# Kernel optimization log

Hardware: AMD Instinct MI355X
Metric: run time of the kernel (lower is better)

The kernel has to match this reference:

```python
import jax, jax.numpy as jnp
import numpy as np

NUM_HEADS = 32
HEAD_DIM = 128
ROPE_DIM = 64
HIDDEN = 4096
C_KV = 512
C_Q = 1536
CACHE_LEN = 4096
BATCH = 4


def _apply_rope(x, positions):
    # x: [B, S, H, R]; interleaved rotate-half RoPE at given absolute positions
    R = x.shape[-1]
    inv_freq = 1.0 / (10000.0 ** (jnp.arange(0, R, 2, dtype=jnp.float32) / R))
    ang = positions[:, None].astype(jnp.float32) * inv_freq[None, :]  # [S, R/2]
    cos = jnp.cos(ang)[None, :, None, :]
    sin = jnp.sin(ang)[None, :, None, :]
    x1, x2 = x[..., 0::2], x[..., 1::2]
    out = jnp.stack([x1 * cos - x2 * sin, x1 * sin + x2 * cos], axis=-1)
    return out.reshape(x.shape).astype(x.dtype)


def setup_inputs() -> dict:
    key = jax.random.key(0)
    ks = jax.random.split(key, 12)
    s = lambda fan: 1.0 / np.sqrt(fan)
    return {
        "hidden_states": jax.random.normal(ks[0], (BATCH, 1, HIDDEN), jnp.float32),
        "mask": jnp.zeros((BATCH, 1, 1, CACHE_LEN + 1), jnp.float32),
        "cached_c_KV": jax.random.normal(ks[1], (BATCH, CACHE_LEN, C_KV), jnp.float32),
        "cached_k_R": jax.random.normal(ks[2], (BATCH, CACHE_LEN, ROPE_DIM), jnp.float32),
        "W_DKV": jax.random.normal(ks[3], (HIDDEN, C_KV), jnp.float32) * s(HIDDEN),
        "W_UK": jax.random.normal(ks[4], (C_KV, NUM_HEADS * HEAD_DIM), jnp.float32) * s(C_KV),
        "W_UV": jax.random.normal(ks[5], (C_KV, NUM_HEADS * HEAD_DIM), jnp.float32) * s(C_KV),
        "W_DQ": jax.random.normal(ks[6], (HIDDEN, C_Q), jnp.float32) * s(HIDDEN),
        "W_UQ": jax.random.normal(ks[7], (C_Q, NUM_HEADS * HEAD_DIM), jnp.float32) * s(C_Q),
        "W_QR": jax.random.normal(ks[8], (C_Q, NUM_HEADS * ROPE_DIM), jnp.float32) * s(C_Q),
        "W_KR": jax.random.normal(ks[9], (HIDDEN, ROPE_DIM), jnp.float32) * s(HIDDEN),
        "W_O": jax.random.normal(ks[10], (NUM_HEADS * HEAD_DIM, HIDDEN), jnp.float32) * s(NUM_HEADS * HEAD_DIM),
    }


def reference(hidden_states, mask, cached_c_KV, cached_k_R,
              W_DKV, W_UK, W_UV, W_DQ, W_UQ, W_QR, W_KR, W_O):
    B = hidden_states.shape[0]
    S_cache = cached_c_KV.shape[1]
    scale = 1.0 / np.sqrt(HEAD_DIM + ROPE_DIM)

    # latent projections for current token
    c_KV = hidden_states @ W_DKV                      # [B,1,C_KV]
    k_C = (c_KV @ W_UK).reshape(B, 1, NUM_HEADS, HEAD_DIM)
    v_C = (c_KV @ W_UV).reshape(B, 1, NUM_HEADS, HEAD_DIM)
    c_Q = hidden_states @ W_DQ                        # [B,1,C_Q]
    q_C = (c_Q @ W_UQ).reshape(B, 1, NUM_HEADS, HEAD_DIM)
    q_R = (c_Q @ W_QR).reshape(B, 1, NUM_HEADS, ROPE_DIM)
    k_R = (hidden_states @ W_KR).reshape(B, 1, 1, ROPE_DIM)

    # RoPE at the current decode position (= cache length)
    pos = jnp.array([S_cache], dtype=jnp.int32)
    q_R = _apply_rope(q_R, pos)
    k_R_cur = _apply_rope(k_R, pos)
    k_R_cur = jnp.broadcast_to(k_R_cur, (B, 1, NUM_HEADS, ROPE_DIM))

    q = jnp.concatenate([q_C, q_R], axis=-1)          # [B,1,H,D+R]
    k_cur = jnp.concatenate([k_C, k_R_cur], axis=-1)  # [B,1,H,D+R]

    # re-up-project cached latents (the expensive MLA decode step)
    cached_k_C = (cached_c_KV @ W_UK).reshape(B, S_cache, NUM_HEADS, HEAD_DIM)
    cached_v_C = (cached_c_KV @ W_UV).reshape(B, S_cache, NUM_HEADS, HEAD_DIM)
    cached_k_R_exp = jnp.broadcast_to(cached_k_R[:, :, None, :],
                                      (B, S_cache, NUM_HEADS, ROPE_DIM))
    cached_k = jnp.concatenate([cached_k_C, cached_k_R_exp], axis=-1)

    k = jnp.concatenate([cached_k, k_cur], axis=1)    # [B,S+1,H,D+R]
    v = jnp.concatenate([cached_v_C, v_C], axis=1)    # [B,S+1,H,D]

    # single-query attention: scores [B,H,1,S+1]
    scores = jnp.einsum('bqhd,bkhd->bhqk', q, k) * scale
    scores = scores + mask * -1e9
    probs = jax.nn.softmax(scores, axis=-1)
    attn = jnp.einsum('bhqk,bkhd->bqhd', probs, v).reshape(B, 1, NUM_HEADS * HEAD_DIM)

    out = attn @ W_O                                  # [B,1,HIDDEN]
    new_cached_c_KV = jnp.concatenate([cached_c_KV, c_KV], axis=1)
    new_cached_k_R = jnp.concatenate([cached_k_R, k_R_cur[:, :, 0, :]], axis=1)
    return out, new_cached_c_KV, new_cached_k_R
```

## Files before the change

kernel.cpp:

```cpp
#include <hip/hip_runtime.h>
#include <math.h>

#define NB 4
#define HID 4096
#define CKV 512
#define CQ 1536
#define NH 32
#define HD 128
#define RD 64
#define SS 4096
#define SK 4097
#define SKP 4100

#define SCALE_F 0.07216878364870322f

#define NP1 64
#define NP2 24
#define NPV 32
#define NUV 16
#define NWO 32

#define KD   576
#define QKB_STR 584
#define PBF_STR 4104

typedef __attribute__((ext_vector_type(8))) short short8v;
typedef __attribute__((ext_vector_type(4))) float f32x4;

enum : int {
  WS_QABS  = 0,
  WS_QROPE = WS_QABS + NB*NH*CKV,
  WS_KROPE = WS_QROPE + NB*NH*RD,
  WS_CKV   = WS_KROPE + NB*RD,
  WS_CQ    = WS_CKV + NB*CKV,
  WS_SCA   = WS_CQ + NB*CQ,
  WS_P1    = WS_SCA + NB*NH*SKP,
  WS_P2    = WS_P1 + NP1*NB*528*4,
  WS_OPART = WS_P2 + NP2*NB*6144,
  WS_UVPART= WS_OPART + NPV*NB*NH*CKV,
  WS_WOPART= WS_UVPART + NUV*NB*HID,
  WS_KVBF  = WS_WOPART + NWO*NB*HID,
  WS_QBF   = WS_KVBF + (NB*SK*KD)/2,
  WS_PBF   = WS_QBF + (NB*NH*KD)/2,
  WS_TOTAL = WS_PBF + (NB*NH*PBF_STR)/2
};

__device__ inline void fma4(float4& a, float s, const float4& v) {
  a.x += s*v.x; a.y += s*v.y; a.z += s*v.z; a.w += s*v.w;
}
__device__ inline float dot4(const float4& a, const float4& b) {
  return a.x*b.x + a.y*b.y + a.z*b.z + a.w*b.w;
}
__device__ inline unsigned short f2bf(float f) {
  union { float f; unsigned int u; } v; v.f = f;
  unsigned int r = v.u + 0x7FFFu + ((v.u >> 16) & 1u);
  return (unsigned short)(r >> 16);
}
__device__ inline ushort4 f2bf4(float4 v) {
  ushort4 r; r.x = f2bf(v.x); r.y = f2bf(v.y); r.z = f2bf(v.z); r.w = f2bf(v.w);
  return r;
}
__device__ inline float bf2f(unsigned short u) {
  union { unsigned int u; float f; } v; v.u = ((unsigned int)u) << 16;
  return v.f;
}
__device__ inline float4 bf2f4(ushort4 u) {
  float4 r; r.x = bf2f(u.x); r.y = bf2f(u.y); r.z = bf2f(u.z); r.w = bf2f(u.w);
  return r;
}

__global__ __launch_bounds__(256)
void k_proj1copy(const float* __restrict__ hidden,
                 const float* __restrict__ Wdkv,
                 const float* __restrict__ Wdq,
                 const float* __restrict__ Wkr,
                 float* __restrict__ ws,
                 const float4* __restrict__ src_ckv,
                 const float4* __restrict__ src_kr,
                 float4* __restrict__ dst_ckv,
                 float4* __restrict__ dst_kr) {
  __shared__ float4 red_s[4][NB][64];
  unsigned short* kvbf = (unsigned short*)(ws + WS_KVBF);
  const int bx = blockIdx.x;
  if (bx < 576) {
    const int gx = bx % 9, gy = bx / 9;
    const int lane = threadIdx.x & 63, ksub = threadIdx.x >> 6;
    const int col4 = gx * 64 + lane;
    const int k0 = gy * 64 + ksub * 16;
    const bool valid = col4 < 528;
    float4 acc[NB] = {};
    if (valid) {
      const float* W; int C4, wcol4;
      if (col4 < 128)      { W = Wdkv; C4 = 128; wcol4 = col4; }
      else if (col4 < 512) { W = Wdq;  C4 = 384; wcol4 = col4 - 128; }
      else                 { W = Wkr;  C4 = 16;  wcol4 = col4 - 512; }
      const float4* wp = (const float4*)W + (size_t)k0 * C4 + wcol4;
      #pragma unroll
      for (int i = 0; i < 16; ++i) {
        float4 w4 = wp[(size_t)i * C4];
        #pragma unroll
        for (int b = 0; b < NB; ++b) fma4(acc[b], hidden[b*HID + k0 + i], w4);
      }
    }
    #pragma unroll
    for (int b = 0; b < NB; ++b) red_s[ksub][b][lane] = acc[b];
    __syncthreads();
    if (ksub == 0 && valid) {
      #pragma unroll
      for (int b = 0; b < NB; ++b) {
        float4 s = red_s[0][b][lane];
        #pragma unroll
        for (int j = 1; j < 4; ++j) {
          float4 v = red_s[j][b][lane];
          s.x += v.x; s.y += v.y; s.z += v.z; s.w += v.w;
        }
        *(float4*)(ws + WS_P1 + ((size_t)(gy*NB + b)*528 + col4)*4) = s;
      }
    }
  } else {
    const int bxc = bx - 576;
    if (bxc < 8192) {
      int b = bxc >> 11;
      int idx = (bxc & 2047) * 256 + threadIdx.x;
      float4 v = src_ckv[(size_t)b*(SS*CKV/4) + idx];
      dst_ckv[(size_t)b*(SK*CKV/4) + idx] = v;
      int off = idx * 4;
      int k = off >> 9, c = off & 511;
      *(ushort4*)(kvbf + ((size_t)b*SK + k)*KD + c) = f2bf4(v);
    } else {
      int bx2 = bxc - 8192;
      int b = bx2 >> 8;
      int idx = (bx2 & 255) * 256 + threadIdx.x;
      float4 v = src_kr[(size_t)b*(SS*RD/4) + idx];
      dst_kr[(size_t)b*(SK*RD/4) + idx] = v;
      int off = idx * 4;
      int k = off >> 6, rr = off & 63;
      *(ushort4*)(kvbf + ((size_t)b*SK + k)*KD + 512 + rr) = f2bf4(v);
    }
  }
}

__global__ __launch_bounds__(256)
void k_proj2r1(const float* __restrict__ Wuq,
               const float* __restrict__ Wqr,
               float* __restrict__ ws,
               float* __restrict__ out_ckv,
               float* __restrict__ out_kr) {
  __shared__ float4 red_s[4][NB][64];
  __shared__ float act_s[NB][64];
  unsigned short* kvbf = (unsigned short*)(ws + WS_KVBF);
  const int bx = blockIdx.x;
  const int tid = threadIdx.x;
  if (bx < 576) {
    const int gx = bx % 24, gy = bx / 24;
    {
      const int b = tid >> 6, i = tid & 63;
      const int k = gy * 64 + i;
      const float* base = ws + WS_P1 + (size_t)b*2112 + 512 + k;
      float s = 0.f;
      #pragma unroll 8
      for (int p = 0; p < NP1; ++p) s += base[(size_t)p*NB*2112];
      act_s[b][i] = s;
    }
    __syncthreads();
    const int lane = tid & 63, ksub = tid >> 6;
    const int col4 = gx * 64 + lane;
    const float* W; int C4, wcol4;
    if (col4 < 1024) { W = Wuq; C4 = 1024; wcol4 = col4; }
    else             { W = Wqr; C4 = 512;  wcol4 = col4 - 1024; }
    const float4* wp = (const float4*)W + (size_t)(gy*64 + ksub*16) * C4 + wcol4;
    float4 acc[NB] = {};
    #pragma unroll
    for (int i = 0; i < 16; ++i) {
      float4 w4 = wp[(size_t)i * C4];
      #pragma unroll
      for (int b = 0; b < NB; ++b) fma4(acc[b], act_s[b][ksub*16 + i], w4);
    }
    #pragma unroll
    for (int b = 0; b < NB; ++b) red_s[ksub][b][lane] = acc[b];
    __syncthreads();
    if (ksub == 0) {
      #pragma unroll
      for (int b = 0; b < NB; ++b) {
        float4 s = red_s[0][b][lane];
        #pragma unroll
        for (int j = 1; j < 4; ++j) {
          float4 v = red_s[j][b][lane];
          s.x += v.x; s.y += v.y; s.z += v.z; s.w += v.w;
        }
        *(float4*)(ws + WS_P2 + (size_t)(gy*NB + b)*6144 + col4*4) = s;
      }
    }
  } else {
    const int w = (bx - 576) * 256 + tid;
    if (w >= 528*NB) return;
    const int b = w / 528, col4 = w % 528;
    float4 s = {};
    #pragma unroll 8
    for (int p = 0; p < NP1; ++p) {
      float4 v = *(const float4*)(ws + WS_P1 + ((size_t)(p*NB + b)*528 + col4)*4);
      s.x += v.x; s.y += v.y; s.z += v.z; s.w += v.w;
    }
    if (col4 < 128) {
      *(float4*)(ws + WS_CKV + b*CKV + col4*4) = s;
      *(float4*)(out_ckv + (size_t)b*SK*CKV + (size_t)SS*CKV + col4*4) = s;
      *(ushort4*)(kvbf + ((size_t)b*SK + SS)*KD + col4*4) = f2bf4(s);
    } else if (col4 < 512) {
      *(float4*)(ws + WS_CQ + b*CQ + (col4 - 128)*4) = s;
    } else {
      const int c0 = (col4 - 512) * 4;
      const double LN1E4 = 9.210340371976184;
      int i0 = c0 >> 1;
      double a0 = 4096.0 * exp(-(double)i0 / 32.0 * LN1E4);
      double a1 = 4096.0 * exp(-(double)(i0 + 1) / 32.0 * LN1E4);
      float c0f = (float)cos(a0), s0f = (float)sin(a0);
      float c1f = (float)cos(a1), s1f = (float)sin(a1);
      float4 o;
      o.x = s.x*c0f - s.y*s0f;  o.y = s.x*s0f + s.y*c0f;
      o.z = s.z*c1f - s.w*s1f;  o.w = s.z*s1f + s.w*c1f;
      *(float4*)(ws + WS_KROPE + b*RD + c0) = o;
      *(float4*)(out_kr + (size_t)b*SK*RD + (size_t)SS*RD + c0) = o;
      *(ushort4*)(kvbf + ((size_t)b*SK + SS)*KD + 512 + c0) = f2bf4(o);
    }
  }
}

__global__ __launch_bounds__(256)
void k_absorb_rope(const float* __restrict__ Wuk,
                   float* __restrict__ ws) {
  unsigned short* qbf = (unsigned short*)(ws + WS_QBF);
  const int bid = blockIdx.x, tid = threadIdx.x;
  if (bid < 256) {
    const int h = bid >> 3, cq = bid & 7;
    __shared__ float qc_s[NB][HD];
    __shared__ float part_s[NB][256];
    for (int e = tid; e < NB*HD; e += 256) {
      int b = e >> 7, d = e & 127;
      float v = 0.f;
      #pragma unroll
      for (int p = 0; p < NP2; ++p)
        v += ws[WS_P2 + (size_t)(p*NB + b)*6144 + h*HD + d];
      qc_s[b][d] = v;
    }
    __syncthreads();
    const int c = cq*64 + (tid & 63);
    const int dg = tid >> 6;
    const float4* wrow = (const float4*)(Wuk + (size_t)c*(NH*HD) + h*HD + dg*32);
    float acc[NB] = {0,0,0,0};
    #pragma unroll
    for (int d4 = 0; d4 < 8; ++d4) {
      float4 w4 = wrow[d4];
      #pragma unroll
      for (int b = 0; b < NB; ++b)
        acc[b] += dot4(w4, *(const float4*)&qc_s[b][dg*32 + d4*4]);
    }
    #pragma unroll
    for (int b = 0; b < NB; ++b) part_s[b][tid] = acc[b];
    __syncthreads();
    if (tid < 64) {
      #pragma unroll
      for (int b = 0; b < NB; ++b) {
        float v = (part_s[b][tid] + part_s[b][tid+64] + part_s[b][tid+128] + part_s[b][tid+192]) * SCALE_F;
        ws[WS_QABS + (size_t)(b*NH + h)*CKV + cq*64 + tid] = v;
        qbf[(size_t)(b*NH + h)*KD + cq*64 + tid] = f2bf(v);
      }
    }
  } else {
    const int b = bid - 256;
    const double LN1E4 = 9.210340371976184;
    for (int pid = tid; pid < NH*32; pid += 256) {
      int h = pid >> 5, i = pid & 31;
      float x1 = 0.f, x2 = 0.f;
      #pragma unroll
      for (int p = 0; p < NP2; ++p) {
        const float* base = ws + WS_P2 + (size_t)(p*NB + b)*6144 + 4096 + h*RD + 2*i;
        x1 += base[0]; x2 += base[1];
      }
      double ang = 4096.0 * exp(-(double)i / 32.0 * LN1E4);
      float cs = (float)cos(ang), sn = (float)sin(ang);
      float o0 = (x1*cs - x2*sn) * SCALE_F;
      float o1 = (x1*sn + x2*cs) * SCALE_F;
      ws[WS_QROPE + (b*NH + h)*RD + 2*i]     = o0;
      ws[WS_QROPE + (b*NH + h)*RD + 2*i + 1] = o1;
      qbf[(size_t)(b*NH + h)*KD + 512 + 2*i]     = f2bf(o0);
      qbf[(size_t)(b*NH + h)*KD + 512 + 2*i + 1] = f2bf(o1);
    }
  }
}

__global__ __launch_bounds__(256)
void k_scores_mfma(float* __restrict__ ws) {
  __shared__ unsigned short q_s[32 * QKB_STR];
  __shared__ unsigned short kv_s[32 * QKB_STR];
  const unsigned short* kvbf = (const unsigned short*)(ws + WS_KVBF);
  const unsigned short* qbf  = (const unsigned short*)(ws + WS_QBF);
  const int tid = threadIdx.x;
  const int b  = blockIdx.y;
  const int k0 = blockIdx.x * 32;
  {
    const int r = tid >> 3, u0 = tid & 7;
    const unsigned short* qsrc = qbf + (size_t)(b*NH + r)*KD;
    const int k = k0 + r;
    const unsigned short* ksrc = (k <= SS) ? (kvbf + ((size_t)b*SK + k)*KD) : nullptr;
    #pragma unroll
    for (int j = 0; j < 9; ++j) {
      int u = (u0 + 8*j) * 8;
      *(uint4*)&q_s[r*QKB_STR + u] = *(const uint4*)(qsrc + u);
      uint4 kvv = {0u, 0u, 0u, 0u};
      if (ksrc) kvv = *(const uint4*)(ksrc + u);
      *(uint4*)&kv_s[r*QKB_STR + u] = kvv;
    }
  }
  __syncthreads();
  const int wid = tid >> 6, lane = tid & 63;
  const int m0 = (wid & 1) * 16;
  const int n0 = (wid >> 1) * 16;
  const int l15 = lane & 15, lq = lane >> 4;
  const unsigned short* arow = &q_s[(m0 + l15)*QKB_STR + lq*8];
  const unsigned short* brow = &kv_s[(n0 + l15)*QKB_STR + lq*8];
  f32x4 acc = {0.f, 0.f, 0.f, 0.f};
  #pragma unroll
  for (int ks = 0; ks < 18; ++ks) {
    short8v a = *(const short8v*)(arow + ks*32);
    short8v bb = *(const short8v*)(brow + ks*32);
    acc = __builtin_amdgcn_mfma_f32_16x16x32_bf16(a, bb, acc, 0, 0, 0);
  }
  const int key = k0 + n0 + l15;
  if (key <= SS) {
    #pragma unroll
    for (int r = 0; r < 4; ++r) {
      int h = m0 + lq*4 + r;
      ws[WS_SCA + (size_t)(b*NH + h)*SKP + key] = acc[r];
    }
  }
}

__global__ __launch_bounds__(256)
void k_softmax(const float* __restrict__ mask, float* __restrict__ ws) {
  __shared__ float red[256];
  unsigned short* pbf = (unsigned short*)(ws + WS_PBF);
  const int tid = threadIdx.x;
  const int b = blockIdx.x >> 5;
  const float* sa = ws + WS_SCA + (size_t)blockIdx.x * SKP;
  unsigned short* prow = pbf + (size_t)blockIdx.x * PBF_STR;
  const float* mrow = mask + (size_t)b * SK;
  float v[17];
  float m = -INFINITY;
  #pragma unroll
  for (int r = 0; r < 17; ++r) {
    int k = tid + r*256;
    v[r] = (k < SK) ? (sa[k] + mrow[k] * (-1e9f)) : -INFINITY;
    m = fmaxf(m, v[r]);
  }
  red[tid] = m; __syncthreads();
  for (int st = 128; st > 0; st >>= 1) {
    if (tid < st) red[tid] = fmaxf(red[tid], red[tid+st]);
    __syncthreads();
  }
  m = red[0]; __syncthreads();
  float e[17];
  float l = 0.f;
  #pragma unroll
  for (int r = 0; r < 17; ++r) {
    int k = tid + r*256;
    e[r] = (k < SK) ? __expf(v[r] - m) : 0.f;
    l += e[r];
  }
  red[tid] = l; __syncthreads();
  for (int st = 128; st > 0; st >>= 1) {
    if (tid < st) red[tid] += red[tid+st];
    __syncthreads();
  }
  float inv = 1.f / red[0];
  #pragma unroll
  for (int r = 0; r < 17; ++r) {
    int k = tid + r*256;
    if (k < SK) prow[k] = f2bf(e[r] * inv);
  }
}

__global__ __launch_bounds__(256)
void k_pv(float* __restrict__ ws) {
  __shared__ float p_s[32][132];
  const unsigned short* kvbf = (const unsigned short*)(ws + WS_KVBF);
  const unsigned short* pbf  = (const unsigned short*)(ws + WS_PBF);
  const int tid = threadIdx.x;
  const int c4 = tid & 15, hg = tid >> 4;
  const int b  = blockIdx.z;
  const int c  = blockIdx.y * 64 + c4 * 4;
  const int k0 = blockIdx.x * 128;
  #pragma unroll
  for (int j = 0; j < 2; ++j) {
    int u = tid + j*256;
    int h = u >> 4, c8 = u & 15;
    const unsigned short* src = pbf + (size_t)(b*NH + h)*PBF_STR + k0 + c8*8;
    ushort4 a0 = *(const ushort4*)(src);
    ushort4 a1 = *(const ushort4*)(src + 4);
    float4 f0 = bf2f4(a0), f1 = bf2f4(a1);
    *(float4*)&p_s[h][c8*8]     = f0;
    *(float4*)&p_s[h][c8*8 + 4] = f1;
  }
  __syncthreads();
  const unsigned short* kvp = kvbf + ((size_t)b*SK + k0)*KD + c;
  float4 acc0 = {}, acc1 = {};
  #pragma unroll 4
  for (int kk = 0; kk < 128; kk += 4) {
    float4 kv4[4];
    #pragma unroll
    for (int j = 0; j < 4; ++j)
      kv4[j] = bf2f4(*(const ushort4*)(kvp + (size_t)(kk + j)*KD));
    float4 p4a = *(const float4*)&p_s[hg][kk];
    float4 p4b = *(const float4*)&p_s[hg + 16][kk];
    fma4(acc0, p4a.x, kv4[0]); fma4(acc1, p4b.x, kv4[0]);
    fma4(acc0, p4a.y, kv4[1]); fma4(acc1, p4b.y, kv4[1]);
    fma4(acc0, p4a.z, kv4[2]); fma4(acc1, p4b.z, kv4[2]);
    fma4(acc0, p4a.w, kv4[3]); fma4(acc1, p4b.w, kv4[3]);
  }
  if (blockIdx.x == NPV - 1) {
    float4 kv = bf2f4(*(const ushort4*)(kvbf + ((size_t)b*SK + SS)*KD + c));
    float pa = bf2f(pbf[(size_t)(b*NH + hg)*PBF_STR + SS]);
    float pb = bf2f(pbf[(size_t)(b*NH + hg + 16)*PBF_STR + SS]);
    fma4(acc0, pa, kv);
    fma4(acc1, pb, kv);
  }
  *(float4*)(ws + WS_OPART + (((size_t)blockIdx.x*NB + b)*NH + hg)*CKV + c) = acc0;
  *(float4*)(ws + WS_OPART + (((size_t)blockIdx.x*NB + b)*NH + hg + 16)*CKV + c) = acc1;
}

__global__ __launch_bounds__(256)
void k_uv2(const float* __restrict__ Wuv, float* __restrict__ ws) {
  __shared__ float4 red_s[4][NB][64];
  __shared__ float ol_s[NB][2][32];
  const int tid = threadIdx.x;
  const int x = blockIdx.x & 15, y = blockIdx.x >> 4;
  {
    const int b = tid >> 6, hh = (tid >> 5) & 1, ci = tid & 31;
    const float* base = ws + WS_OPART + ((size_t)b*NH + (2*x + hh))*CKV + y*32 + ci;
    float s = 0.f;
    #pragma unroll 8
    for (int p = 0; p < NPV; ++p) s += base[(size_t)p*(NB*NH*CKV)];
    ol_s[b][hh][ci] = s;
  }
  __syncthreads();
  const int lane = tid & 63, csub = tid >> 6;
  const int col4 = x * 64 + lane;
  const int hh = (col4 >> 5) & 1;
  const float4* wp = (const float4*)Wuv + (size_t)(y*32 + csub*8) * 1024 + col4;
  float4 acc[NB] = {};
  #pragma unroll
  for (int i = 0; i < 8; ++i) {
    float4 w4 = wp[(size_t)i * 1024];
    #pragma unroll
    for (int b = 0; b < NB; ++b)
      fma4(acc[b], ol_s[b][hh][csub*8 + i], w4);
  }
  #pragma unroll
  for (int b = 0; b < NB; ++b) red_s[csub][b][lane] = acc[b];
  __syncthreads();
  if (csub == 0) {
    #pragma unroll
    for (int b = 0; b < NB; ++b) {
      float4 s = red_s[0][b][lane];
      #pragma unroll
      for (int j = 1; j < 4; ++j) {
        float4 v = red_s[j][b][lane];
        s.x += v.x; s.y += v.y; s.z += v.z; s.w += v.w;
      }
      *(float4*)(ws + WS_UVPART + (size_t)(y*NB + b)*HID + col4*4) = s;
    }
  }
}

__global__ __launch_bounds__(256)
void k_wo2(const float* __restrict__ Wo, float* __restrict__ ws) {
  __shared__ float4 red_s[4][NB][64];
  __shared__ float at_s[NB][128];
  const int tid = threadIdx.x;
  const int x = blockIdx.x & 15, y = blockIdx.x >> 4;
  {
    const int b = tid >> 6, q = tid & 63;
    #pragma unroll
    for (int e = 0; e < 2; ++e) {
      int idx = q*2 + e;
      const float* base = ws + WS_UVPART + (size_t)b*HID + y*128 + idx;
      float s = 0.f;
      #pragma unroll
      for (int p = 0; p < NUV; ++p) s += base[(size_t)p*(NB*HID)];
      at_s[b][idx] = s;
    }
  }
  __syncthreads();
  const int lane = tid & 63, ksub = tid >> 6;
  const int col4 = x * 64 + lane;
  const float4* wp = (const float4*)Wo + (size_t)(y*128 + ksub*32) * 1024 + col4;
  float4 acc[NB] = {};
  #pragma unroll 8
  for (int i = 0; i < 32; ++i) {
    float4 w4 = wp[(size_t)i * 1024];
    #pragma unroll
    for (int b = 0; b < NB; ++b)
      fma4(acc[b], at_s[b][ksub*32 + i], w4);
  }
  #pragma unroll
  for (int b = 0; b < NB; ++b) red_s[ksub][b][lane] = acc[b];
  __syncthreads();
  if (ksub == 0) {
    #pragma unroll
    for (int b = 0; b < NB; ++b) {
      float4 s = red_s[0][b][lane];
      #pragma unroll
      for (int j = 1; j < 4; ++j) {
        float4 v = red_s[j][b][lane];
        s.x += v.x; s.y += v.y; s.z += v.z; s.w += v.w;
      }
      *(float4*)(ws + WS_WOPART + (size_t)(y*NB + b)*HID + col4*4) = s;
    }
  }
}

__global__ __launch_bounds__(256)
void k_reduce5(const float* __restrict__ ws, float* __restrict__ out) {
  const int idx = blockIdx.x * 256 + threadIdx.x;
  float4 s = {};
  #pragma unroll 8
  for (int p = 0; p < NWO; ++p) {
    float4 v = *(const float4*)(ws + WS_WOPART + (size_t)p*(NB*HID) + (size_t)idx*4);
    s.x += v.x; s.y += v.y; s.z += v.z; s.w += v.w;
  }
  *(float4*)(out + (size_t)idx*4) = s;
}

extern "C" void kernel_launch(void* const* d_in, const int* in_sizes, int n_in,
                              void* d_out, int out_size, void* d_ws, size_t ws_size,
                              hipStream_t stream) {
  (void)in_sizes; (void)n_in; (void)out_size; (void)ws_size;
  const float* hidden = (const float*)d_in[0];
  const float* mask   = (const float*)d_in[1];
  const float* ckv_c  = (const float*)d_in[2];
  const float* kr_c   = (const float*)d_in[3];
  const float* Wdkv   = (const float*)d_in[4];
  const float* Wuk    = (const float*)d_in[5];
  const float* Wuv    = (const float*)d_in[6];
  const float* Wdq    = (const float*)d_in[7];
  const float* Wuq    = (const float*)d_in[8];
  const float* Wqr    = (const float*)d_in[9];
  const float* Wkr    = (const float*)d_in[10];
  const float* Wo     = (const float*)d_in[11];
  float* out = (float*)d_out;
  float* ws  = (float*)d_ws;
  float* out_ckv = out + NB*HID;
  float* out_kr  = out + NB*HID + (size_t)NB*SK*CKV;

  k_proj1copy<<<9792, 256, 0, stream>>>(hidden, Wdkv, Wdq, Wkr, ws,
                                        (const float4*)ckv_c, (const float4*)kr_c,
                                        (float4*)out_ckv, (float4*)out_kr);
  k_proj2r1<<<585, 256, 0, stream>>>(Wuq, Wqr, ws, out_ckv, out_kr);
  k_absorb_rope<<<260, 256, 0, stream>>>(Wuk, ws);
  k_scores_mfma<<<dim3(129, 4), 256, 0, stream>>>(ws);
  k_softmax<<<NB*NH, 256, 0, stream>>>(mask, ws);
  k_pv<<<dim3(NPV, 8, 4), 256, 0, stream>>>(ws);
  k_uv2<<<256, 256, 0, stream>>>(Wuv, ws);
  k_wo2<<<512, 256, 0, stream>>>(Wo, ws);
  k_reduce5<<<16, 256, 0, stream>>>(ws, out);
}
```

Baseline: 110.7 us.

## Rewrite PV stage with bf16 MFMA and read Q directly from global in scores

The probabilities-times-latent-values stage moves from scalar FP32 FMAs to bf16 MFMA 16x16x32 tiles. Each chunk of KV is transposed into LDS so the B operand can be loaded as contiguous vectors, and the launch grid is halved along the channel dimension. The extra last-token term moves into the k_uv2 reduction. The scores kernel also stops staging Q in shared memory and loads the A operand straight from global memory. The cost is per-element transposed LDS stores that may cause bank conflicts, and uncached global loads for Q.

```diff
diff --git a/kernel.cpp b/kernel.cpp
--- a/kernel.cpp
+++ b/kernel.cpp
@@ -23,6 +23,7 @@
 #define KD   576
 #define QKB_STR 584
 #define PBF_STR 4104
+#define TV_STR 40
 
 typedef __attribute__((ext_vector_type(8))) short short8v;
 typedef __attribute__((ext_vector_type(4))) float f32x4;
@@ -290,7 +291,6 @@
 
 __global__ __launch_bounds__(256)
 void k_scores_mfma(float* __restrict__ ws) {
-  __shared__ unsigned short q_s[32 * QKB_STR];
   __shared__ unsigned short kv_s[32 * QKB_STR];
   const unsigned short* kvbf = (const unsigned short*)(ws + WS_KVBF);
   const unsigned short* qbf  = (const unsigned short*)(ws + WS_QBF);
@@ -299,13 +299,11 @@
   const int k0 = blockIdx.x * 32;
   {
     const int r = tid >> 3, u0 = tid & 7;
-    const unsigned short* qsrc = qbf + (size_t)(b*NH + r)*KD;
     const int k = k0 + r;
     const unsigned short* ksrc = (k <= SS) ? (kvbf + ((size_t)b*SK + k)*KD) : nullptr;
     #pragma unroll
     for (int j = 0; j < 9; ++j) {
       int u = (u0 + 8*j) * 8;
-      *(uint4*)&q_s[r*QKB_STR + u] = *(const uint4*)(qsrc + u);
       uint4 kvv = {0u, 0u, 0u, 0u};
       if (ksrc) kvv = *(const uint4*)(ksrc + u);
       *(uint4*)&kv_s[r*QKB_STR + u] = kvv;
@@ -316,7 +314,7 @@
   const int m0 = (wid & 1) * 16;
   const int n0 = (wid >> 1) * 16;
   const int l15 = lane & 15, lq = lane >> 4;
-  const unsigned short* arow = &q_s[(m0 + l15)*QKB_STR + lq*8];
+  const unsigned short* arow = qbf + (size_t)(b*NH + m0 + l15)*KD + lq*8;
   const unsigned short* brow = &kv_s[(n0 + l15)*QKB_STR + lq*8];
   f32x4 acc = {0.f, 0.f, 0.f, 0.f};
   #pragma unroll
@@ -380,65 +378,78 @@
 }
 
 __global__ __launch_bounds__(256)
-void k_pv(float* __restrict__ ws) {
-  __shared__ float p_s[32][132];
+void k_pv_mfma(float* __restrict__ ws) {
+  __shared__ unsigned short kvT_s[128 * TV_STR];
   const unsigned short* kvbf = (const unsigned short*)(ws + WS_KVBF);
   const unsigned short* pbf  = (const unsigned short*)(ws + WS_PBF);
   const int tid = threadIdx.x;
-  const int c4 = tid & 15, hg = tid >> 4;
   const int b  = blockIdx.z;
-  const int c  = blockIdx.y * 64 + c4 * 4;
+  const int c0 = blockIdx.y * 128;
   const int k0 = blockIdx.x * 128;
-  #pragma unroll
-  for (int j = 0; j < 2; ++j) {
-    int u = tid + j*256;
-    int h = u >> 4, c8 = u & 15;
-    const unsigned short* src = pbf + (size_t)(b*NH + h)*PBF_STR + k0 + c8*8;
-    ushort4 a0 = *(const ushort4*)(src);
-    ushort4 a1 = *(const ushort4*)(src + 4);
-    float4 f0 = bf2f4(a0), f1 = bf2f4(a1);
-    *(float4*)&p_s[h][c8*8]     = f0;
-    *(float4*)&p_s[h][c8*8 + 4] = f1;
-  }
-  __syncthreads();
-  const unsigned short* kvp = kvbf + ((size_t)b*SK + k0)*KD + c;
-  float4 acc0 = {}, acc1 = {};
-  #pragma unroll 4
-  for (int kk = 0; kk < 128; kk += 4) {
-    float4 kv4[4];
-    #pragma unroll
-    for (int j = 0; j < 4; ++j)
-      kv4[j] = bf2f4(*(const ushort4*)(kvp + (size_t)(kk + j)*KD));
-    float4 p4a = *(const float4*)&p_s[hg][kk];
-    float4 p4b = *(const float4*)&p_s[hg + 16][kk];
-    fma4(acc0, p4a.x, kv4[0]); fma4(acc1, p4b.x, kv4[0]);
-    fma4(acc0, p4a.y, kv4[1]); fma4(acc1, p4b.y, kv4[1]);
-    fma4(acc0, p4a.z, kv4[2]); fma4(acc1, p4b.z, kv4[2]);
-    fma4(acc0, p4a.w, kv4[3]); fma4(acc1, p4b.w, kv4[3]);
-  }
-  if (blockIdx.x == NPV - 1) {
-    float4 kv = bf2f4(*(const ushort4*)(kvbf + ((size_t)b*SK + SS)*KD + c));
-    float pa = bf2f(pbf[(size_t)(b*NH + hg)*PBF_STR + SS]);
-    float pb = bf2f(pbf[(size_t)(b*NH + hg + 16)*PBF_STR + SS]);
-    fma4(acc0, pa, kv);
-    fma4(acc1, pb, kv);
-  }
-  *(float4*)(ws + WS_OPART + (((size_t)blockIdx.x*NB + b)*NH + hg)*CKV + c) = acc0;
-  *(float4*)(ws + WS_OPART + (((size_t)blockIdx.x*NB + b)*NH + hg + 16)*CKV + c) = acc1;
+  const int wid = tid >> 6, lane = tid & 63;
+  const int l15 = lane & 15, lq = lane >> 4;
+  const int m0 = (wid & 1) * 16;
+  const int nq = (wid >> 1) * 4;
+  f32x4 acc[4] = {{0,0,0,0},{0,0,0,0},{0,0,0,0},{0,0,0,0}};
+  const int kk_st = tid & 31, cgrp = tid >> 5;
+  #pragma unroll
+  for (int sc = 0; sc < 4; ++sc) {
+    const int ks0 = k0 + sc*32;
+    {
+      const unsigned short* src = kvbf + ((size_t)b*SK + ks0 + kk_st)*KD + c0 + cgrp*16;
+      #pragma unroll
+      for (int half = 0; half < 2; ++half) {
+        ushort4 v0 = *(const ushort4*)(src + half*8);
+        ushort4 v1 = *(const ushort4*)(src + half*8 + 4);
+        int cb = cgrp*16 + half*8;
+        kvT_s[(cb+0)*TV_STR + kk_st] = v0.x;
+        kvT_s[(cb+1)*TV_STR + kk_st] = v0.y;
+        kvT_s[(cb+2)*TV_STR + kk_st] = v0.z;
+        kvT_s[(cb+3)*TV_STR + kk_st] = v0.w;
+        kvT_s[(cb+4)*TV_STR + kk_st] = v1.x;
+        kvT_s[(cb+5)*TV_STR + kk_st] = v1.y;
+        kvT_s[(cb+6)*TV_STR + kk_st] = v1.z;
+        kvT_s[(cb+7)*TV_STR + kk_st] = v1.w;
+      }
+    }
+    __syncthreads();
+    short8v a = *(const short8v*)(pbf + (size_t)(b*NH + m0 + l15)*PBF_STR + ks0 + lq*8);
+    #pragma unroll
+    for (int nt = 0; nt < 4; ++nt) {
+      const unsigned short* brow = &kvT_s[((nq + nt)*16 + l15)*TV_STR + lq*8];
+      short8v bb = *(const short8v*)(brow);
+      acc[nt] = __builtin_amdgcn_mfma_f32_16x16x32_bf16(a, bb, acc[nt], 0, 0, 0);
+    }
+    __syncthreads();
+  }
+  #pragma unroll
+  for (int nt = 0; nt < 4; ++nt) {
+    const int c = c0 + (nq + nt)*16 + l15;
+    #pragma unroll
+    for (int r = 0; r < 4; ++r) {
+      int h = m0 + lq*4 + r;
+      ws[WS_OPART + (((size_t)blockIdx.x*NB + b)*NH + h)*CKV + c] = acc[nt][r];
+    }
+  }
 }
 
 __global__ __launch_bounds__(256)
 void k_uv2(const float* __restrict__ Wuv, float* __restrict__ ws) {
   __shared__ float4 red_s[4][NB][64];
   __shared__ float ol_s[NB][2][32];
+  const unsigned short* kvbf = (const unsigned short*)(ws + WS_KVBF);
+  const unsigned short* pbf  = (const unsigned short*)(ws + WS_PBF);
   const int tid = threadIdx.x;
   const int x = blockIdx.x & 15, y = blockIdx.x >> 4;
   {
     const int b = tid >> 6, hh = (tid >> 5) & 1, ci = tid & 31;
-    const float* base = ws + WS_OPART + ((size_t)b*NH + (2*x + hh))*CKV + y*32 + ci;
+    const int h = 2*x + hh, c = y*32 + ci;
+    const float* base = ws + WS_OPART + ((size_t)b*NH + h)*CKV + c;
     float s = 0.f;
     #pragma unroll 8
     for (int p = 0; p < NPV; ++p) s += base[(size_t)p*(NB*NH*CKV)];
+    s += bf2f(pbf[(size_t)(b*NH + h)*PBF_STR + SS]) *
+         bf2f(kvbf[((size_t)b*SK + SS)*KD + c]);
     ol_s[b][hh][ci] = s;
   }
   __syncthreads();
@@ -558,7 +569,7 @@
   k_absorb_rope<<<260, 256, 0, stream>>>(Wuk, ws);
   k_scores_mfma<<<dim3(129, 4), 256, 0, stream>>>(ws);
   k_softmax<<<NB*NH, 256, 0, stream>>>(mask, ws);
-  k_pv<<<dim3(NPV, 8, 4), 256, 0, stream>>>(ws);
+  k_pv_mfma<<<dim3(NPV, 4, 4), 256, 0, stream>>>(ws);
   k_uv2<<<256, 256, 0, stream>>>(Wuv, ws);
   k_wo2<<<512, 256, 0, stream>>>(Wo, ws);
   k_reduce5<<<16, 256, 0, stream>>>(ws, out);
```

Result: faster. 99.94 us (-9.7%).
